# Performance work log

Measured on AMD Instinct MI355X. Metric: run time of the kernel, lower is better.

Reference implementation:

```python
import jax, jax.numpy as jnp
import numpy as np

B, T, H, M = 16, 1024, 512, 80
NHEADS, HDIM = 8, H // 8


def _p(key, shape, scale=0.05):
    return scale * jax.random.normal(key, shape, dtype=jnp.float32)


def setup_inputs() -> dict:
    key = jax.random.key(0)
    ks = jax.random.split(key, 20)
    return {
        "encoder_memory": jax.random.normal(ks[0], (B, T, H), dtype=jnp.float32),
        "target_mel": jax.random.normal(ks[1], (B, T, M), dtype=jnp.float32),
        # prenet Linear(mel_dim -> hidden_dim)
        "w_prenet": _p(ks[2], (H, M)), "b_prenet": _p(ks[3], (H,)),
        # MultiheadAttention packed in-proj (3H, H) and out-proj (H, H)
        "in_proj_w": _p(ks[4], (3 * H, H)), "in_proj_b": _p(ks[5], (3 * H,)),
        "out_proj_w": _p(ks[6], (H, H)), "out_proj_b": _p(ks[7], (H,)),
        # 2-layer LSTM (torch gate order i,f,g,o); h0=c0=0 each step so W_hh acts on zeros
        "w_ih0": _p(ks[8], (4 * H, 2 * H)), "w_hh0": _p(ks[9], (4 * H, H)),
        "b_ih0": _p(ks[10], (4 * H,)), "b_hh0": _p(ks[11], (4 * H,)),
        "w_ih1": _p(ks[12], (4 * H, H)), "w_hh1": _p(ks[13], (4 * H, H)),
        "b_ih1": _p(ks[14], (4 * H,)), "b_hh1": _p(ks[15], (4 * H,)),
        # mel projection Linear(hidden_dim -> mel_dim)
        "w_mel": _p(ks[16], (M, H)), "b_mel": _p(ks[17], (M,)),
    }


def _lstm_cell_zero_state(x, w_ih, w_hh, b_ih, b_hh):
    # single step from zero (h, c): the W_hh @ h0 term is exactly zero
    gates = x @ w_ih.T + (b_ih + b_hh)  # (B,T,4H)
    i, f, g, o = jnp.split(gates, 4, axis=-1)
    c = jax.nn.sigmoid(i) * jnp.tanh(g)  # f * c_prev == 0
    return jax.nn.sigmoid(o) * jnp.tanh(c)


def reference(encoder_memory, target_mel, w_prenet, b_prenet,
              in_proj_w, in_proj_b, out_proj_w, out_proj_b,
              w_ih0, w_hh0, b_ih0, b_hh0, w_ih1, w_hh1, b_ih1, b_hh1,
              w_mel, b_mel):
    # teacher forcing: prev_mel at step t is zeros (t=0) else target_mel[:, t-1]
    prev = jnp.concatenate(
        [jnp.zeros((B, 1, M), dtype=target_mel.dtype), target_mel[:, :-1]], axis=1)
    pre = jax.nn.relu(prev @ w_prenet.T + b_prenet)  # (B,T,H); dropout is identity (eval)

    # cross-attention: each step's length-1 query attends over all encoder frames,
    # which vectorizes to standard (no-mask) MHA with queries = pre
    wq, wk, wv = jnp.split(in_proj_w, 3, axis=0)
    bq, bk, bv = jnp.split(in_proj_b, 3, axis=0)
    q = (pre @ wq.T + bq).reshape(B, T, NHEADS, HDIM)
    k = (encoder_memory @ wk.T + bk).reshape(B, T, NHEADS, HDIM)
    v = (encoder_memory @ wv.T + bv).reshape(B, T, NHEADS, HDIM)
    scale = 1.0 / jnp.sqrt(jnp.float32(HDIM))
    scores = jnp.einsum('bqhd,bkhd->bhqk', q * scale, k)  # (B,8,T,T)
    attn = jax.nn.softmax(scores, axis=-1)
    ctx = jnp.einsum('bhqk,bkhd->bqhd', attn, v).reshape(B, T, H)
    attn_out = ctx @ out_proj_w.T + out_proj_b  # (B,T,H)

    dec_in = jnp.concatenate([pre, attn_out], axis=-1)  # (B,T,2H)
    h1 = _lstm_cell_zero_state(dec_in, w_ih0, w_hh0, b_ih0, b_hh0)
    h2 = _lstm_cell_zero_state(h1, w_ih1, w_hh1, b_ih1, b_hh1)
    return h2 @ w_mel.T + b_mel  # (B,T,M)
```

## Files before the change

### kernel.cpp

```cpp
#include <hip/hip_runtime.h>


typedef _Float16 f16;
typedef _Float16 f16x8 __attribute__((ext_vector_type(8)));
typedef _Float16 f16x4 __attribute__((ext_vector_type(4)));
typedef float f32x4 __attribute__((ext_vector_type(4)));

constexpr int B_ = 16, T_ = 1024, H_ = 512, M_ = 80;
constexpr int NH_ = 8, D_ = 64;
constexpr int N_ = B_ * T_;

#define MFMA16(a, b, c) __builtin_amdgcn_mfma_f32_16x16x32_f16(a, b, c, 0, 0, 0)

__device__ __forceinline__ void gload_lds16(const f16* g, f16* l) {
  __builtin_amdgcn_global_load_lds(
      (const __attribute__((address_space(1))) void*)g,
      (__attribute__((address_space(3))) void*)l, 16, 0, 0);
}

__device__ __forceinline__ float fexp2(float x) {
#if __has_builtin(__builtin_amdgcn_exp2f)
  return __builtin_amdgcn_exp2f(x);
#else
  return exp2f(x);
#endif
}

template <int EPI, bool CONCATA, bool NCHK>
__global__ __launch_bounds__(256) void mgemm(
    const f16* __restrict__ A, const f16* __restrict__ A2,
    const f16* __restrict__ Wt, const float* __restrict__ bias,
    const float* __restrict__ bias2, float scale, void* __restrict__ outp,
    int K, int N) {
  __shared__ f16 As[128 * 64];
  __shared__ f16 Bs[128 * 64];
  const int tid = threadIdx.x;
  const int lane = tid & 63, wid = tid >> 6;
  const int lq = lane & 15, lg = lane >> 4;
  const int wm = wid >> 1, wn = wid & 1;
  const int r0 = blockIdx.x * 128, c0 = blockIdx.y * 128;

  f32x4 acc[4][4] = {};

  for (int k0 = 0; k0 < K; k0 += 64) {
#pragma unroll
    for (int it = 0; it < 4; ++it) {
      const int off = it * 4096 + wid * 1024 + lane * 16;
      const int row = off >> 7;
      const int cb = (off >> 4) & 7;
      const int kc = k0 + ((cb ^ (row & 7)) << 3);
      const f16* src;
      if (CONCATA) {
        src = (kc < 512) ? (A + (size_t)(r0 + row) * 512 + kc)
                         : (A2 + (size_t)(r0 + row) * 512 + (kc - 512));
      } else {
        src = A + (size_t)(r0 + row) * K + kc;
      }
      gload_lds16(src, (f16*)((char*)As + off));
    }
#pragma unroll
    for (int it = 0; it < 4; ++it) {
      const int off = it * 4096 + wid * 1024 + lane * 16;
      const int row = off >> 7;
      const int cb = (off >> 4) & 7;
      int crow = c0 + row;
      if (NCHK) crow = crow < N ? crow : N - 1;
      gload_lds16(Wt + (size_t)crow * K + k0 + ((cb ^ (row & 7)) << 3),
                  (f16*)((char*)Bs + off));
    }
    __syncthreads();
#pragma unroll
    for (int kk = 0; kk < 2; ++kk) {
      f16x8 af[4], bf[4];
#pragma unroll
      for (int m = 0; m < 4; ++m) {
        const int row = wm * 64 + m * 16 + lq;
        af[m] = *(const f16x8*)((const char*)As + row * 128 +
                                (((kk * 4 + lg) ^ (row & 7)) << 4));
      }
#pragma unroll
      for (int n = 0; n < 4; ++n) {
        const int row = wn * 64 + n * 16 + lq;
        bf[n] = *(const f16x8*)((const char*)Bs + row * 128 +
                                (((kk * 4 + lg) ^ (row & 7)) << 4));
      }
#pragma unroll
      for (int m = 0; m < 4; ++m)
#pragma unroll
        for (int n = 0; n < 4; ++n) acc[m][n] = MFMA16(af[m], bf[n], acc[m][n]);
    }
    __syncthreads();
  }

#pragma unroll
  for (int m = 0; m < 4; ++m) {
    const int rbase = r0 + wm * 64 + m * 16 + lg * 4;
#pragma unroll
    for (int n = 0; n < 4; ++n) {
      const int col = c0 + wn * 64 + n * 16 + lq;
      if (NCHK && col >= N) continue;
      const float bsum = bias[col] + (bias2 ? bias2[col] : 0.f);
      const f32x4 a = acc[m][n];
      if (EPI == 3) {
        const int b = rbase >> 10, t = rbase & (T_ - 1);
        const int head = col >> 6, d = col & 63;
        f16x4 pk;
#pragma unroll
        for (int r = 0; r < 4; ++r) pk[r] = (f16)((a[r] + bsum) * scale);
        *(f16x4*)((f16*)outp + ((size_t)((b * NH_ + head) * D_ + d)) * T_ + t) =
            pk;
      } else {
#pragma unroll
        for (int r = 0; r < 4; ++r) {
          const int row = rbase + r;
          float v = (a[r] + bsum) * scale;
          if (EPI == 1) v = fmaxf(v, 0.f);
          if (EPI == 4)
            ((float*)outp)[(size_t)row * N + col] = v;
          else
            ((f16*)outp)[(size_t)row * N + col] = (f16)v;
        }
      }
    }
  }
}

template <bool CONCATA>
__global__ __launch_bounds__(256, 2) void lstm_fused(
    const f16* __restrict__ A, const f16* __restrict__ A2,
    const f16* __restrict__ Wih, const float* __restrict__ bih,
    const float* __restrict__ bhh, f16* __restrict__ Hout_) {
  constexpr int K = CONCATA ? 1024 : 512;
  __shared__ f16 As[128 * 64];
  __shared__ f16 Bs[3][128 * 64];
  const int tid = threadIdx.x;
  const int lane = tid & 63, wid = tid >> 6;
  const int lq = lane & 15, lg = lane >> 4;
  const int wm = wid >> 1, wn = wid & 1;
  const int r0 = blockIdx.x * 128, c0 = blockIdx.y * 128;

  f32x4 acc[3][4][4] = {};

  for (int k0 = 0; k0 < K; k0 += 64) {
#pragma unroll
    for (int it = 0; it < 4; ++it) {
      const int off = it * 4096 + tid * 16;
      const int row = off >> 7;
      const int cb = (off >> 4) & 7;
      const int kc = k0 + ((cb ^ (row & 7)) << 3);
      const f16* src;
      if (CONCATA) {
        src = (kc < 512) ? (A + (size_t)(r0 + row) * 512 + kc)
                         : (A2 + (size_t)(r0 + row) * 512 + (kc - 512));
      } else {
        src = A + (size_t)(r0 + row) * K + kc;
      }
      gload_lds16(src, (f16*)((char*)As + off));
    }
#pragma unroll
    for (int g = 0; g < 3; ++g) {
      const int gbase = (g == 0) ? 0 : 512 * (g + 1);
#pragma unroll
      for (int it = 0; it < 4; ++it) {
        const int off = it * 4096 + tid * 16;
        const int row = off >> 7;
        const int cb = (off >> 4) & 7;
        gload_lds16(
            Wih + (size_t)(gbase + c0 + row) * K + k0 + ((cb ^ (row & 7)) << 3),
            (f16*)((char*)&Bs[g][0] + off));
      }
    }
    __syncthreads();
#pragma unroll
    for (int kk = 0; kk < 2; ++kk) {
      f16x8 af[4];
#pragma unroll
      for (int m = 0; m < 4; ++m) {
        const int row = wm * 64 + m * 16 + lq;
        af[m] = *(const f16x8*)((const char*)As + row * 128 +
                                (((kk * 4 + lg) ^ (row & 7)) << 4));
      }
#pragma unroll
      for (int g = 0; g < 3; ++g)
#pragma unroll
        for (int n = 0; n < 4; ++n) {
          const int row = wn * 64 + n * 16 + lq;
          const f16x8 bf = *(const f16x8*)((const char*)&Bs[g][0] + row * 128 +
                                           (((kk * 4 + lg) ^ (row & 7)) << 4));
#pragma unroll
          for (int m = 0; m < 4; ++m)
            acc[g][m][n] = MFMA16(af[m], bf, acc[g][m][n]);
        }
    }
    __syncthreads();
  }

#pragma unroll
  for (int n = 0; n < 4; ++n) {
    const int c = c0 + wn * 64 + n * 16 + lq;
    const float bi = bih[c] + bhh[c];
    const float bg = bih[1024 + c] + bhh[1024 + c];
    const float bo = bih[1536 + c] + bhh[1536 + c];
#pragma unroll
    for (int m = 0; m < 4; ++m) {
      const int rbase = r0 + wm * 64 + m * 16 + lg * 4;
#pragma unroll
      for (int r = 0; r < 4; ++r) {
        const float gi = acc[0][m][n][r] + bi;
        const float gg = acc[1][m][n][r] + bg;
        const float go = acc[2][m][n][r] + bo;
        const float si = 1.f / (1.f + __expf(-gi));
        const float so = 1.f / (1.f + __expf(-go));
        const float tg = 2.f / (1.f + __expf(-2.f * gg)) - 1.f;
        const float cc = si * tg;
        const float tc = 2.f / (1.f + __expf(-2.f * cc)) - 1.f;
        Hout_[(size_t)(rbase + r) * 512 + c] = (f16)(so * tc);
      }
    }
  }
}

__global__ __launch_bounds__(256, 2) void kv_fused(
    const f16* __restrict__ A, const f16* __restrict__ Wt,
    const float* __restrict__ bias, f16* __restrict__ kout,
    f16* __restrict__ vout) {
  constexpr int K = 512;
  __shared__ f16 As[128 * 64];
  __shared__ f16 Bs[2][128 * 64];
  const int tid = threadIdx.x;
  const int lane = tid & 63, wid = tid >> 6;
  const int lq = lane & 15, lg = lane >> 4;
  const int wm = wid >> 1, wn = wid & 1;
  const int r0 = blockIdx.x * 128, c0 = blockIdx.y * 128;

  f32x4 acc[2][4][4] = {};

  for (int k0 = 0; k0 < K; k0 += 64) {
#pragma unroll
    for (int it = 0; it < 4; ++it) {
      const int off = it * 4096 + tid * 16;
      const int row = off >> 7;
      const int cb = (off >> 4) & 7;
      const int kc = k0 + ((cb ^ (row & 7)) << 3);
      gload_lds16(A + (size_t)(r0 + row) * K + kc, (f16*)((char*)As + off));
    }
#pragma unroll
    for (int g = 0; g < 2; ++g) {
#pragma unroll
      for (int it = 0; it < 4; ++it) {
        const int off = it * 4096 + tid * 16;
        const int row = off >> 7;
        const int cb = (off >> 4) & 7;
        gload_lds16(
            Wt + (size_t)(g * 512 + c0 + row) * K + k0 + ((cb ^ (row & 7)) << 3),
            (f16*)((char*)&Bs[g][0] + off));
      }
    }
    __syncthreads();
#pragma unroll
    for (int kk = 0; kk < 2; ++kk) {
      f16x8 af[4];
#pragma unroll
      for (int m = 0; m < 4; ++m) {
        const int row = wm * 64 + m * 16 + lq;
        af[m] = *(const f16x8*)((const char*)As + row * 128 +
                                (((kk * 4 + lg) ^ (row & 7)) << 4));
      }
#pragma unroll
      for (int g = 0; g < 2; ++g)
#pragma unroll
        for (int n = 0; n < 4; ++n) {
          const int row = wn * 64 + n * 16 + lq;
          const f16x8 bf = *(const f16x8*)((const char*)&Bs[g][0] + row * 128 +
                                           (((kk * 4 + lg) ^ (row & 7)) << 4));
#pragma unroll
          for (int m = 0; m < 4; ++m)
            acc[g][m][n] = MFMA16(af[m], bf, acc[g][m][n]);
        }
    }
    __syncthreads();
  }

#pragma unroll
  for (int m = 0; m < 4; ++m) {
    const int rbase = r0 + wm * 64 + m * 16 + lg * 4;
    const int b = rbase >> 10, t = rbase & (T_ - 1);
#pragma unroll
    for (int n = 0; n < 4; ++n) {
      const int col = c0 + wn * 64 + n * 16 + lq;
      const float bk = bias[col];
#pragma unroll
      for (int r = 0; r < 4; ++r)
        kout[(size_t)(rbase + r) * 512 + col] = (f16)(acc[0][m][n][r] + bk);
      const float bv = bias[512 + col];
      const int head = col >> 6, d = col & 63;
      f16x4 pk;
#pragma unroll
      for (int r = 0; r < 4; ++r) pk[r] = (f16)(acc[1][m][n][r] + bv);
      *(f16x4*)(vout + ((size_t)((b * NH_ + head) * D_ + d)) * T_ + t) = pk;
    }
  }
}

__global__ __launch_bounds__(256) void attn_mfma6(
    const f16* __restrict__ q, const f16* __restrict__ k,
    const f16* __restrict__ vT, f16* __restrict__ ctx) {
  __shared__ f16 Ks[2][64 * 64];
  __shared__ f16 Vs[2][64 * 64];
  __shared__ f16 Ps[4][16 * 64];
  const int bid = blockIdx.x;
  const int nid = (bid & 7) * 128 + (bid >> 3);
  const int qt = nid & 7, bh = nid >> 3;
  const int head = bh & 7, b = bh >> 3;
  const int tid = threadIdx.x, lane = tid & 63, wid = tid >> 6;
  const int lq = lane & 15, lg = lane >> 4;

  const f16* kbase = k + ((size_t)b * T_) * H_ + head * D_;
  const f16* vbase = vT + (size_t)bh * D_ * T_;

  auto stage = [&](int kt, int buf) {
#pragma unroll
    for (int it = 0; it < 2; ++it) {
      const int off = it * 4096 + tid * 16;
      const int row = off >> 7;
      const int sc = ((((off >> 4) & 7) ^ (row & 7)) << 3);
      gload_lds16(kbase + (size_t)(kt * 64 + row) * H_ + sc,
                  (f16*)((char*)&Ks[buf][0] + off));
      gload_lds16(vbase + (size_t)row * T_ + kt * 64 + sc,
                  (f16*)((char*)&Vs[buf][0] + off));
    }
  };

  const int q0 = qt * 128 + wid * 32;
  f16x8 qf[2][2];
#pragma unroll
  for (int s = 0; s < 2; ++s)
#pragma unroll
    for (int kk = 0; kk < 2; ++kk)
      qf[s][kk] = *(const f16x8*)(q + ((size_t)(b * T_) + q0 + s * 16 + lq) * H_ +
                                  head * D_ + kk * 32 + lg * 8);

  f16x8 ones;
#pragma unroll
  for (int j = 0; j < 8; ++j) ones[j] = (f16)1.f;

  f32x4 accO[2][4] = {};
  f32x4 accL[2] = {};
  char* pw = (char*)&Ps[wid][0] + lq * 128;
  const int psw = (lq & 7) << 4;

  stage(0, 0);
  __syncthreads();

  for (int kt = 0; kt < T_ / 64; ++kt) {
    const int cur = kt & 1;
    if (kt < T_ / 64 - 1) stage(kt + 1, cur ^ 1);

    f16x8 kf[4][2];
#pragma unroll
    for (int n = 0; n < 4; ++n)
#pragma unroll
      for (int kk = 0; kk < 2; ++kk) {
        const int row = n * 16 + lq;
        kf[n][kk] = *(const f16x8*)((const char*)&Ks[cur][0] + row * 128 +
                                    (((kk * 4 + lg) ^ (row & 7)) << 4));
      }
    f32x4 ssw[2][4] = {};
    __builtin_amdgcn_s_setprio(1);
#pragma unroll
    for (int s = 0; s < 2; ++s)
#pragma unroll
      for (int n = 0; n < 4; ++n)
#pragma unroll
        for (int kk = 0; kk < 2; ++kk)
          ssw[s][n] = MFMA16(kf[n][kk], qf[s][kk], ssw[s][n]);
    __builtin_amdgcn_s_setprio(0);

    f16x8 vf[4][2];
#pragma unroll
    for (int n = 0; n < 4; ++n)
#pragma unroll
      for (int kk = 0; kk < 2; ++kk) {
        const int row = n * 16 + lq;
        vf[n][kk] = *(const f16x8*)((const char*)&Vs[cur][0] + row * 128 +
                                    (((kk * 4 + lg) ^ (row & 7)) << 4));
      }

#pragma unroll
    for (int s = 0; s < 2; ++s) {
#pragma unroll
      for (int n = 0; n < 4; ++n) {
        f16x4 pk;
#pragma unroll
        for (int r = 0; r < 4; ++r) pk[r] = (f16)fexp2(ssw[s][n][r]);
        *(f16x4*)(pw + ((n * 32 + lg * 8) ^ psw)) = pk;
      }
      f16x8 pb[2];
#pragma unroll
      for (int kk = 0; kk < 2; ++kk)
        pb[kk] = *(const f16x8*)(pw + ((((kk * 4 + lg) << 4)) ^ psw));
      __builtin_amdgcn_s_setprio(1);
#pragma unroll
      for (int kk = 0; kk < 2; ++kk) {
        accL[s] = MFMA16(ones, pb[kk], accL[s]);
#pragma unroll
        for (int n = 0; n < 4; ++n)
          accO[s][n] = MFMA16(vf[n][kk], pb[kk], accO[s][n]);
      }
      __builtin_amdgcn_s_setprio(0);
    }
    __syncthreads();
  }

#pragma unroll
  for (int s = 0; s < 2; ++s) {
    const float inv = 1.f / accL[s][0];
    const size_t rowoff = ((size_t)(b * T_) + q0 + s * 16 + lq) * H_ + head * D_;
#pragma unroll
    for (int n = 0; n < 4; ++n) {
      f16x4 o;
#pragma unroll
      for (int r = 0; r < 4; ++r) o[r] = (f16)(accO[s][n][r] * inv);
      *(f16x4*)(ctx + rowoff + n * 16 + lg * 4) = o;
    }
  }
}

constexpr int C0 = 2097152;
constexpr int C1 = C0 + 196608;
constexpr int C2 = C1 + 65536;
constexpr int C3 = C2 + 524288;
constexpr int C4 = C3 + 262144;
constexpr int C5 = C4 + 10240;
constexpr int C6 = C5 + 524288;
constexpr int C7 = C6 + 16384;
__global__ void conv_all(const float* __restrict__ enc, const float* __restrict__ inw,
                         const float* __restrict__ outw, const float* __restrict__ wih0,
                         const float* __restrict__ wih1, const float* __restrict__ wmel,
                         const float* __restrict__ tmel, const float* __restrict__ wpre,
                         f16* denc, f16* dinw, f16* doutw, f16* dwih0,
                         f16* dwih1, f16* dwmel, f16* dpm, f16* dwp) {
  const int i = blockIdx.x * blockDim.x + threadIdx.x;
  if (i >= C7) return;
  if (i < C5) {
    const float* s;
    f16* d;
    int off;
    if (i < C0) { s = enc; d = denc; off = i; }
    else if (i < C1) { s = inw; d = dinw; off = i - C0; }
    else if (i < C2) { s = outw; d = doutw; off = i - C1; }
    else if (i < C3) { s = wih0; d = dwih0; off = i - C2; }
    else if (i < C4) { s = wih1; d = dwih1; off = i - C3; }
    else { s = wmel; d = dwmel; off = i - C4; }
    const float4 v = ((const float4*)s)[off];
    f16x4 o = {(f16)v.x, (f16)v.y, (f16)v.z, (f16)v.w};
    ((f16x4*)d)[off] = o;
  } else if (i < C6) {
    const int j = i - C5;
    const int r = j >> 5, c4 = (j & 31) * 4;
    const int t = r & (T_ - 1);
    f16x4 o = {};
    if (t != 0 && c4 < M_) {
      const float4 v = *(const float4*)(tmel + (size_t)(r - 1) * M_ + c4);
      o = {(f16)v.x, (f16)v.y, (f16)v.z, (f16)v.w};
    }
    *(f16x4*)(dpm + (size_t)r * 128 + c4) = o;
  } else {
    const int j = i - C6;
    const int r = j >> 5, c4 = (j & 31) * 4;
    f16x4 o = {};
    if (c4 < M_) {
      const float4 v = *(const float4*)(wpre + (size_t)r * M_ + c4);
      o = {(f16)v.x, (f16)v.y, (f16)v.z, (f16)v.w};
    }
    *(f16x4*)(dwp + (size_t)r * 128 + c4) = o;
  }
}

extern "C" void kernel_launch(void* const* d_in, const int* in_sizes, int n_in,
                              void* d_out, int out_size, void* d_ws,
                              size_t ws_size, hipStream_t stream) {
  const float* enc = (const float*)d_in[0];
  const float* tmel = (const float*)d_in[1];
  const float* w_pre = (const float*)d_in[2];
  const float* b_pre = (const float*)d_in[3];
  const float* inw = (const float*)d_in[4];
  const float* inb = (const float*)d_in[5];
  const float* outw = (const float*)d_in[6];
  const float* outb = (const float*)d_in[7];
  const float* wih0 = (const float*)d_in[8];
  const float* bih0 = (const float*)d_in[10];
  const float* bhh0 = (const float*)d_in[11];
  const float* wih1 = (const float*)d_in[12];
  const float* bih1 = (const float*)d_in[14];
  const float* bhh1 = (const float*)d_in[15];
  const float* wmel = (const float*)d_in[16];
  const float* bmel = (const float*)d_in[17];

  f16* wsh = (f16*)d_ws;
  const size_t SEG = (size_t)N_ * H_;
  f16* EncB = wsh;
  f16* h1 = wsh + SEG;
  f16* pre = wsh + 2 * SEG;
  f16* qb = wsh + 3 * SEG;
  f16* kbuf = wsh + 4 * SEG;
  f16* vTb = wsh + 5 * SEG;
  f16* ctx = wsh + 6 * SEG;
  f16* aout = EncB;
  f16* h2 = qb;
  f16* WP = wsh + 7 * SEG;
  f16* WIN = WP + 512 * 128;
  f16* WOUT = WIN + 1536 * 512;
  f16* WIH0 = WOUT + 512 * 512;
  f16* WIH1 = WIH0 + 2048 * 1024;
  f16* WMEL = WIH1 + 2048 * 512;
  f16* PM = WMEL + 80 * 512;

  const dim3 blk(256);
  conv_all<<<(C7 + 255) / 256, blk, 0, stream>>>(
      enc, inw, outw, wih0, wih1, wmel, tmel, w_pre, EncB, WIN, WOUT, WIH0,
      WIH1, WMEL, PM, WP);

  const dim3 g512(N_ / 128, 4), g80(N_ / 128, 1);
  mgemm<1, false, false><<<g512, blk, 0, stream>>>(PM, nullptr, WP, b_pre,
                                                   nullptr, 1.f, pre, 128, 512);
  mgemm<0, false, false><<<g512, blk, 0, stream>>>(
      pre, nullptr, WIN, inb, nullptr, 0.125f * 1.44269504088896f, qb, 512, 512);
  kv_fused<<<g512, blk, 0, stream>>>(EncB, WIN + 512 * 512, inb + 512, kbuf,
                                     vTb);
  attn_mfma6<<<dim3(1024), blk, 0, stream>>>(qb, kbuf, vTb, ctx);
  mgemm<0, false, false><<<g512, blk, 0, stream>>>(ctx, nullptr, WOUT, outb,
                                                   nullptr, 1.f, aout, 512, 512);
  lstm_fused<true><<<g512, blk, 0, stream>>>(pre, aout, WIH0, bih0, bhh0, h1);
  lstm_fused<false><<<g512, blk, 0, stream>>>(h1, nullptr, WIH1, bih1, bhh1, h2);
  mgemm<4, false, true><<<g80, blk, 0, stream>>>(h2, nullptr, WMEL, bmel,
                                                 nullptr, 1.f, (float*)d_out,
                                                 512, 80);
}
```

Before: 264.3 us.

## Fold attention out-projection into LSTM layer-0 input weights

The out-projection is linear, so its weight is pre-multiplied into the attention half of the LSTM layer-0 input weights and its bias is folded into the gate biases. This removes the full N×512×512 out-projection GEMM and the aout round trip through memory, at the cost of a small weight-product GEMM, a transpose and a bias fold run every call. The fused weight is rounded to fp16 after the product, which changes numerics slightly.

```diff
diff --git a/kernel.cpp b/kernel.cpp
--- a/kernel.cpp
+++ b/kernel.cpp
@@ -99,7 +99,8 @@
     for (int n = 0; n < 4; ++n) {
       const int col = c0 + wn * 64 + n * 16 + lq;
       if (NCHK && col >= N) continue;
-      const float bsum = bias[col] + (bias2 ? bias2[col] : 0.f);
+      const float bsum =
+          (EPI == 5) ? 0.f : bias[col] + (bias2 ? bias2[col] : 0.f);
       const f32x4 a = acc[m][n];
       if (EPI == 3) {
         const int b = rbase >> 10, t = rbase & (T_ - 1);
@@ -128,8 +129,9 @@
 template <bool CONCATA>
 __global__ __launch_bounds__(256, 2) void lstm_fused(
     const f16* __restrict__ A, const f16* __restrict__ A2,
-    const f16* __restrict__ Wih, const float* __restrict__ bih,
-    const float* __restrict__ bhh, f16* __restrict__ Hout_) {
+    const f16* __restrict__ Wa, const f16* __restrict__ Wb,
+    const float* __restrict__ bih, const float* __restrict__ bhh,
+    const float* __restrict__ bias3, f16* __restrict__ Hout_) {
   constexpr int K = CONCATA ? 1024 : 512;
   __shared__ f16 As[128 * 64];
   __shared__ f16 Bs[3][128 * 64];
@@ -142,6 +144,8 @@
   f32x4 acc[3][4][4] = {};
 
   for (int k0 = 0; k0 < K; k0 += 64) {
+    const f16* Wsrc = (CONCATA && k0 >= 512) ? Wb : Wa;
+    const int kb = (CONCATA && k0 >= 512) ? k0 - 512 : k0;
 #pragma unroll
     for (int it = 0; it < 4; ++it) {
       const int off = it * 4096 + tid * 16;
@@ -166,7 +170,7 @@
         const int row = off >> 7;
         const int cb = (off >> 4) & 7;
         gload_lds16(
-            Wih + (size_t)(gbase + c0 + row) * K + k0 + ((cb ^ (row & 7)) << 3),
+            Wsrc + (size_t)(gbase + c0 + row) * 512 + kb + ((cb ^ (row & 7)) << 3),
             (f16*)((char*)&Bs[g][0] + off));
       }
     }
@@ -198,9 +202,9 @@
 #pragma unroll
   for (int n = 0; n < 4; ++n) {
     const int c = c0 + wn * 64 + n * 16 + lq;
-    const float bi = bih[c] + bhh[c];
-    const float bg = bih[1024 + c] + bhh[1024 + c];
-    const float bo = bih[1536 + c] + bhh[1536 + c];
+    const float bi = bih[c] + bhh[c] + (bias3 ? bias3[c] : 0.f);
+    const float bg = bih[1024 + c] + bhh[1024 + c] + (bias3 ? bias3[1024 + c] : 0.f);
+    const float bo = bih[1536 + c] + bhh[1536 + c] + (bias3 ? bias3[1536 + c] : 0.f);
 #pragma unroll
     for (int m = 0; m < 4; ++m) {
       const int rbase = r0 + wm * 64 + m * 16 + lg * 4;
@@ -438,23 +442,42 @@
                          const float* __restrict__ outw, const float* __restrict__ wih0,
                          const float* __restrict__ wih1, const float* __restrict__ wmel,
                          const float* __restrict__ tmel, const float* __restrict__ wpre,
-                         f16* denc, f16* dinw, f16* doutw, f16* dwih0,
+                         f16* denc, f16* dinw, f16* dwoT, f16* dwa, f16* dw2,
                          f16* dwih1, f16* dwmel, f16* dpm, f16* dwp) {
   const int i = blockIdx.x * blockDim.x + threadIdx.x;
   if (i >= C7) return;
-  if (i < C5) {
-    const float* s;
-    f16* d;
-    int off;
-    if (i < C0) { s = enc; d = denc; off = i; }
-    else if (i < C1) { s = inw; d = dinw; off = i - C0; }
-    else if (i < C2) { s = outw; d = doutw; off = i - C1; }
-    else if (i < C3) { s = wih0; d = dwih0; off = i - C2; }
-    else if (i < C4) { s = wih1; d = dwih1; off = i - C3; }
-    else { s = wmel; d = dwmel; off = i - C4; }
-    const float4 v = ((const float4*)s)[off];
+  if (i < C0) {
+    const float4 v = ((const float4*)enc)[i];
+    ((f16x4*)denc)[i] = {(f16)v.x, (f16)v.y, (f16)v.z, (f16)v.w};
+  } else if (i < C1) {
+    const int j = i - C0;
+    const float4 v = ((const float4*)inw)[j];
+    ((f16x4*)dinw)[j] = {(f16)v.x, (f16)v.y, (f16)v.z, (f16)v.w};
+  } else if (i < C2) {
+    const int j = i - C1;
+    const int r = j >> 7, c4 = (j & 127) * 4;
+    const float4 v = *(const float4*)(outw + (size_t)r * 512 + c4);
+    dwoT[(size_t)(c4 + 0) * 512 + r] = (f16)v.x;
+    dwoT[(size_t)(c4 + 1) * 512 + r] = (f16)v.y;
+    dwoT[(size_t)(c4 + 2) * 512 + r] = (f16)v.z;
+    dwoT[(size_t)(c4 + 3) * 512 + r] = (f16)v.w;
+  } else if (i < C3) {
+    const int j = i - C2;
+    const int r = j >> 8, c4 = (j & 255) * 4;
+    const float4 v = *(const float4*)(wih0 + (size_t)r * 1024 + c4);
     f16x4 o = {(f16)v.x, (f16)v.y, (f16)v.z, (f16)v.w};
-    ((f16x4*)d)[off] = o;
+    if (c4 < 512)
+      *(f16x4*)(dwa + (size_t)r * 512 + c4) = o;
+    else
+      *(f16x4*)(dw2 + (size_t)r * 512 + (c4 - 512)) = o;
+  } else if (i < C4) {
+    const int j = i - C3;
+    const float4 v = ((const float4*)wih1)[j];
+    ((f16x4*)dwih1)[j] = {(f16)v.x, (f16)v.y, (f16)v.z, (f16)v.w};
+  } else if (i < C5) {
+    const int j = i - C4;
+    const float4 v = ((const float4*)wmel)[j];
+    ((f16x4*)dwmel)[j] = {(f16)v.x, (f16)v.y, (f16)v.z, (f16)v.w};
   } else if (i < C6) {
     const int j = i - C5;
     const int r = j >> 5, c4 = (j & 31) * 4;
@@ -475,6 +498,22 @@
     }
     *(f16x4*)(dwp + (size_t)r * 128 + c4) = o;
   }
+}
+
+__global__ void fold_bias(const float* __restrict__ wih0,
+                          const float* __restrict__ outb,
+                          float* __restrict__ bf) {
+  const int c = blockIdx.x * blockDim.x + threadIdx.x;
+  if (c >= 2048) return;
+  const float* w = wih0 + (size_t)c * 1024 + 512;
+  float s = 0.f;
+#pragma unroll 4
+  for (int j = 0; j < 128; ++j) {
+    const float4 a = ((const float4*)w)[j];
+    const float4 b = ((const float4*)outb)[j];
+    s += a.x * b.x + a.y * b.y + a.z * b.z + a.w * b.w;
+  }
+  bf[c] = s;
 }
 
 extern "C" void kernel_launch(void* const* d_in, const int* in_sizes, int n_in,
@@ -506,20 +545,25 @@
   f16* kbuf = wsh + 4 * SEG;
   f16* vTb = wsh + 5 * SEG;
   f16* ctx = wsh + 6 * SEG;
-  f16* aout = EncB;
   f16* h2 = qb;
   f16* WP = wsh + 7 * SEG;
   f16* WIN = WP + 512 * 128;
-  f16* WOUT = WIN + 1536 * 512;
-  f16* WIH0 = WOUT + 512 * 512;
-  f16* WIH1 = WIH0 + 2048 * 1024;
+  f16* OUTWT = WIN + 1536 * 512;
+  f16* WA0 = OUTWT + 512 * 512;
+  f16* W2C = WA0 + 2048 * 512;
+  f16* WB0 = W2C + 2048 * 512;
+  f16* WIH1 = WB0 + 2048 * 512;
   f16* WMEL = WIH1 + 2048 * 512;
   f16* PM = WMEL + 80 * 512;
+  float* BF = (float*)(PM + (size_t)N_ * 128);
 
   const dim3 blk(256);
   conv_all<<<(C7 + 255) / 256, blk, 0, stream>>>(
-      enc, inw, outw, wih0, wih1, wmel, tmel, w_pre, EncB, WIN, WOUT, WIH0,
-      WIH1, WMEL, PM, WP);
+      enc, inw, outw, wih0, wih1, wmel, tmel, w_pre, EncB, WIN, OUTWT, WA0,
+      W2C, WIH1, WMEL, PM, WP);
+  fold_bias<<<8, blk, 0, stream>>>(wih0, outb, BF);
+  mgemm<5, false, false><<<dim3(16, 4), blk, 0, stream>>>(
+      W2C, nullptr, OUTWT, nullptr, nullptr, 1.f, WB0, 512, 512);
 
   const dim3 g512(N_ / 128, 4), g80(N_ / 128, 1);
   mgemm<1, false, false><<<g512, blk, 0, stream>>>(PM, nullptr, WP, b_pre,
@@ -529,10 +573,10 @@
   kv_fused<<<g512, blk, 0, stream>>>(EncB, WIN + 512 * 512, inb + 512, kbuf,
                                      vTb);
   attn_mfma6<<<dim3(1024), blk, 0, stream>>>(qb, kbuf, vTb, ctx);
-  mgemm<0, false, false><<<g512, blk, 0, stream>>>(ctx, nullptr, WOUT, outb,
-                                                   nullptr, 1.f, aout, 512, 512);
-  lstm_fused<true><<<g512, blk, 0, stream>>>(pre, aout, WIH0, bih0, bhh0, h1);
-  lstm_fused<false><<<g512, blk, 0, stream>>>(h1, nullptr, WIH1, bih1, bhh1, h2);
+  lstm_fused<true><<<g512, blk, 0, stream>>>(pre, ctx, WA0, WB0, bih0, bhh0,
+                                             BF, h1);
+  lstm_fused<false><<<g512, blk, 0, stream>>>(h1, nullptr, WIH1, nullptr, bih1,
+                                              bhh1, nullptr, h2);
   mgemm<4, false, true><<<g80, blk, 0, stream>>>(h2, nullptr, WMEL, bmel,
                                                  nullptr, 1.f, (float*)d_out,
                                                  512, 80);
```

Result: slower. 294.9 us (+11.6%).
